# Optimization experiments

Measured on AMD Instinct MI355X. Metric: run time of the kernel, lower is better.

Reference implementation:

```python
import jax, jax.numpy as jnp
import numpy as np

NUM_EXPERTS = 64
TOP_K = 2
TEMPERATURE = 1.0
MOMENTUM = 0.9


def _l2norm(x, axis=-1):
    # torch F.normalize: x / max(||x||, eps)
    n = jnp.linalg.norm(x, axis=axis, keepdims=True)
    return x / jnp.maximum(n, 1e-12)


def setup_inputs() -> dict:
    key = jax.random.key(0)
    k1, k2 = jax.random.split(key)
    hidden_states = jax.random.normal(k1, (4, 4096, 2048), dtype=jnp.float32)
    centers = _l2norm(jax.random.normal(k2, (NUM_EXPERTS, 2048), dtype=jnp.float32))
    return {"hidden_states": hidden_states, "centers": centers}


def reference(hidden_states, centers):
    B, T, H = hidden_states.shape
    flat = hidden_states.reshape(-1, H).astype(jnp.float32)  # [N, H]
    N = flat.shape[0]

    # cosine-similarity logits
    reps_n = _l2norm(flat)
    centers_n = _l2norm(centers)
    temp = jnp.maximum(jnp.float32(TEMPERATURE), 1e-6)
    logits = (reps_n @ centers_n.T) / temp  # [N, E]

    probs = jax.nn.softmax(logits, axis=-1)
    top_w, top_ids = jax.lax.top_k(probs, TOP_K)  # [N, k]
    top_w = top_w / (jnp.sum(top_w, axis=-1, keepdims=True) + 1e-9)

    # EMA center update from top-1 routed expert (training+update path)
    route = top_ids[:, 0]  # [N]
    sums = jax.ops.segment_sum(flat, route, num_segments=NUM_EXPERTS)  # [E, H]
    counts = jax.ops.segment_sum(jnp.ones((N, 1), jnp.float32), route,
                                 num_segments=NUM_EXPERTS)  # [E, 1]
    means = sums / (counts + 1e-6)
    updated = _l2norm(MOMENTUM * centers + (1.0 - MOMENTUM) * means)
    new_centers = jnp.where(counts > 0, updated, centers)

    top_ids = top_ids.reshape(B, T, TOP_K)
    top_w = top_w.reshape(B, T, TOP_K)
    return top_ids, top_w, new_centers
```

## Files before the change

kernel.cpp:

```cpp
#include <hip/hip_runtime.h>
#include <math.h>

#define NTOK 16384
#define HDIM 2048
#define NEXP 64
#define KK   32
#define TAU  5e-5f
#define MAXB 2048
#define TB   16
#define KPAD 40
#define TPAD 20

typedef __attribute__((ext_vector_type(8))) short short8;
typedef __attribute__((ext_vector_type(4))) float f32x4;
typedef __attribute__((ext_vector_type(2))) unsigned int uint2v;


__global__ __launch_bounds__(256)
void zero_kernel(float* p, int n) {
  int i = blockIdx.x * 256 + threadIdx.x;
  if (i < n) p[i] = 0.0f;
}

__device__ __forceinline__ float block_reduce_sum(float v, float* red) {
  #pragma unroll
  for (int o = 32; o > 0; o >>= 1) v += __shfl_down(v, o, 64);
  int lane = threadIdx.x & 63;
  int wid  = threadIdx.x >> 6;
  if (lane == 0) red[wid] = v;
  __syncthreads();
  float s = red[0] + red[1] + red[2] + red[3];
  __syncthreads();
  return s;
}

__device__ __forceinline__ double block_reduce_sum_f64(double v, double* red) {
  const int tid = threadIdx.x;
  red[tid] = v;
  __syncthreads();
  if (tid < 128) red[tid] += red[tid + 128];
  __syncthreads();
  if (tid < 64)  red[tid] += red[tid + 64];
  __syncthreads();
  double s = 0.0;
  if (tid < 64) {
    s = red[tid];
    #pragma unroll
    for (int o = 32; o > 0; o >>= 1) s += __shfl_down(s, o, 64);
  }
  if (tid == 0) red[0] = s;
  __syncthreads();
  s = red[0];
  __syncthreads();
  return s;
}

__global__ __launch_bounds__(256)
void cnorm_kernel(const float* __restrict__ c, float* __restrict__ inv_nc) {
  __shared__ float red[4];
  int e = blockIdx.x;
  float ss = 0.f;
  #pragma unroll
  for (int j = 0; j < 8; ++j) {
    float v = c[e * HDIM + threadIdx.x + j * 256];
    ss += v * v;
  }
  float tot = block_reduce_sum(ss, red);
  if (threadIdx.x == 0) inv_nc[e] = 1.0f / fmaxf(sqrtf(tot), 1e-12f);
}

__global__ __launch_bounds__(256)
void cprep_kernel(const float* __restrict__ c, float* __restrict__ inv_nc,
                  float* __restrict__ bn, unsigned short* __restrict__ cbh,
                  unsigned short* __restrict__ cbl, int* __restrict__ zr,
                  int* __restrict__ cnt) {
  __shared__ float red[4];
  __shared__ double redd[256];
  __shared__ float s_nc;
  const int e = blockIdx.x;
  const int tid = threadIdx.x;
  if (e == 0 && tid < 128) zr[tid] = 0;
  if (e == 1 && tid < 64)  cnt[tid] = 0;
  const float* cr = c + (size_t)e * HDIM;
  float ss = 0.f;
  double acc = 0.0;
  #pragma unroll
  for (int j = 0; j < 8; ++j) {
    float v = cr[tid + j * 256];
    ss += v * v;
    double dv = (double)v;
    acc += dv * dv;
  }
  float tot = block_reduce_sum(ss, red);
  double cn = block_reduce_sum_f64(acc, redd);
  if (tid == 0) {
    inv_nc[e] = 1.0f / fmaxf(sqrtf(tot), 1e-12f);
    s_nc = (float)fmax(sqrt(cn), 1e-12);
  }
  __syncthreads();
  const double nc = (double)s_nc;
  #pragma unroll
  for (int j = 0; j < 8; ++j) {
    const int k = tid + j * 256;
    const float v = cr[k];
    bn[(size_t)e * HDIM + k] = (float)((double)v / nc);
    unsigned u = __float_as_uint(v);
    unsigned h = u & 0xffff0000u;
    float r = v - __uint_as_float(h);
    cbh[(size_t)e * HDIM + k] = (unsigned short)(u >> 16);
    cbl[(size_t)e * HDIM + k] = (unsigned short)(__float_as_uint(r) >> 16);
  }
}

__device__ __forceinline__ void cvt2(float v0, float v1, unsigned &hi, unsigned &lo) {
  unsigned u0 = __float_as_uint(v0);
  unsigned u1 = __float_as_uint(v1);
  unsigned h0 = u0 & 0xffff0000u;
  unsigned h1 = u1 & 0xffff0000u;
  float r0 = v0 - __uint_as_float(h0);
  float r1 = v1 - __uint_as_float(h1);
  hi = (u0 >> 16) | h1;
  lo = (__float_as_uint(r0) >> 16) | (__float_as_uint(r1) & 0xffff0000u);
}

__global__ __launch_bounds__(128)
void fused_kernel(const float* __restrict__ x,
                  const unsigned short* __restrict__ cbh,
                  const unsigned short* __restrict__ cbl,
                  const float* __restrict__ inv_nc,
                  float* __restrict__ out, int* __restrict__ route,
                  int* __restrict__ nflag, int* __restrict__ flags,
                  int* __restrict__ cursor, int* __restrict__ cnt,
                  int* __restrict__ bucket, int* __restrict__ posa) {
  __shared__ __align__(16) unsigned short Ah[2][TB][KPAD];
  __shared__ __align__(16) unsigned short Al[2][TB][KPAD];
  __shared__ __align__(16) unsigned short Bh[2][NEXP][KPAD];
  __shared__ __align__(16) unsigned short Bl[2][NEXP][KPAD];
  __shared__ float lg[NEXP][TPAD];
  __shared__ float xn_lds[TB];
  __shared__ float snc[NEXP];

  const int tid  = threadIdx.x;
  const int t0   = blockIdx.x * TB;
  const int sr   = tid >> 3;
  const int sq   = (tid & 7) * 4;
  const int er   = tid >> 1;
  const int eq   = (tid & 1) * 16;
  const int lane = tid & 63;
  const int w    = tid >> 6;
  const int eh   = w * 32;
  const int fr   = lane & 15;
  const int fk   = (lane >> 4) * 8;

  if (tid < NEXP) snc[tid] = inv_nc[tid];

  const float*          xptr = x   + (size_t)(t0 + sr) * HDIM + sq;
  const unsigned short* bh_p = cbh + (size_t)er * HDIM + eq;
  const unsigned short* bl_p = cbl + (size_t)er * HDIM + eq;

  f32x4 xp;
  short8 bh0r, bh1r, bl0r, bl1r;
  float nacc = 0.f;

  auto stage = [&](int b) {
    unsigned h01, l01, h23, l23;
    cvt2(xp.x, xp.y, h01, l01);
    cvt2(xp.z, xp.w, h23, l23);
    *(uint2v*)&Ah[b][sr][sq] = (uint2v){h01, h23};
    *(uint2v*)&Al[b][sr][sq] = (uint2v){l01, l23};
    nacc += xp.x*xp.x + xp.y*xp.y + xp.z*xp.z + xp.w*xp.w;
    *(short8*)&Bh[b][er][eq]     = bh0r;
    *(short8*)&Bh[b][er][eq + 8] = bh1r;
    *(short8*)&Bl[b][er][eq]     = bl0r;
    *(short8*)&Bl[b][er][eq + 8] = bl1r;
  };
  auto ldreg = [&](int it) {
    const int o = it * KK;
    xp   = *(const f32x4*)(xptr + o);
    bh0r = *(const short8*)(bh_p + o);
    bh1r = *(const short8*)(bh_p + o + 8);
    bl0r = *(const short8*)(bl_p + o);
    bl1r = *(const short8*)(bl_p + o + 8);
  };

  ldreg(0);
  stage(0);
  ldreg(1);
  __syncthreads();

  f32x4 acc0 = (f32x4){0.f, 0.f, 0.f, 0.f};
  f32x4 acc1 = (f32x4){0.f, 0.f, 0.f, 0.f};

  for (int it = 0; it < 64; ++it) {
    const int cur = it & 1;
    short8 ah  = *(const short8*)&Ah[cur][fr][fk];
    short8 al  = *(const short8*)&Al[cur][fr][fk];
    short8 bh0 = *(const short8*)&Bh[cur][eh + fr][fk];
    short8 bl0 = *(const short8*)&Bl[cur][eh + fr][fk];
    short8 bh1 = *(const short8*)&Bh[cur][eh + 16 + fr][fk];
    short8 bl1 = *(const short8*)&Bl[cur][eh + 16 + fr][fk];
    if (it < 63) {
      stage(cur ^ 1);
      if (it < 62) ldreg(it + 2);
    }
    acc0 = __builtin_amdgcn_mfma_f32_16x16x32_bf16(ah, bh0, acc0, 0, 0, 0);
    acc0 = __builtin_amdgcn_mfma_f32_16x16x32_bf16(ah, bl0, acc0, 0, 0, 0);
    acc0 = __builtin_amdgcn_mfma_f32_16x16x32_bf16(al, bh0, acc0, 0, 0, 0);
    acc1 = __builtin_amdgcn_mfma_f32_16x16x32_bf16(ah, bh1, acc1, 0, 0, 0);
    acc1 = __builtin_amdgcn_mfma_f32_16x16x32_bf16(ah, bl1, acc1, 0, 0, 0);
    acc1 = __builtin_amdgcn_mfma_f32_16x16x32_bf16(al, bh1, acc1, 0, 0, 0);
    __syncthreads();
  }

  float s = nacc;
  s += __shfl_xor(s, 1, 64);
  s += __shfl_xor(s, 2, 64);
  s += __shfl_xor(s, 4, 64);
  if ((tid & 7) == 0) xn_lds[sr] = s;

  const int tb = (lane >> 4) * 4;
  *(f32x4*)&lg[eh + fr][tb]      = acc0;
  *(f32x4*)&lg[eh + 16 + fr][tb] = acc1;
  __syncthreads();

  if (tid < TB) {
    const int t  = tid;
    const int tg = t0 + t;
    const float inv_nx = 1.0f / fmaxf(sqrtf(xn_lds[t]), 1e-12f);
    float m1 = -1e30f, m2 = -1e30f, m3 = -1e30f;
    int i1 = 0, i2 = 0;
    #pragma unroll
    for (int e = 0; e < NEXP; ++e) {
      float l = lg[e][t] * snc[e] * inv_nx;
      if (l > m1)      { m3 = m2; m2 = m1; i2 = i1; m1 = l; i1 = e; }
      else if (l > m2) { m3 = m2; m2 = l; i2 = e; }
      else if (l > m3) { m3 = l; }
    }
    float Z = 0.f;
    #pragma unroll
    for (int e = 0; e < NEXP; ++e)
      Z += expf(lg[e][t] * snc[e] * inv_nx - m1);
    const float p1w = 1.0f / Z;
    const float p2w = expf(m2 - m1) / Z;
    const float s2  = p1w + p2w + 1e-9f;
    out[tg * 2 + 0] = (float)i1;
    out[tg * 2 + 1] = (float)i2;
    out[2 * NTOK + tg * 2 + 0] = p1w / s2;
    out[2 * NTOK + tg * 2 + 1] = p2w / s2;
    route[tg] = i1;
    const int p = atomicAdd(&cursor[i1], 1);
    atomicAdd(&cnt[i1], 1);
    if (p < MAXB) bucket[i1 * MAXB + p] = tg;
    posa[tg] = p;
    if ((m1 - m2) < TAU || (m2 - m3) < TAU) {
      int idx = atomicAdd(nflag, 1);
      flags[idx] = tg;
    }
  }
}

__global__ __launch_bounds__(256)
void refine_np_kernel(const float* __restrict__ x, const float* __restrict__ bn,
                      float* __restrict__ out, int* __restrict__ route,
                      const int* __restrict__ nflag, const int* __restrict__ flags,
                      int* __restrict__ cursor, int* __restrict__ cnt,
                      int* __restrict__ bucket, int* __restrict__ posa) {
  __shared__ float a_lds[HDIM];
  __shared__ double redd[256];
  __shared__ float lf[NEXP];
  __shared__ float s_nx;
  const int tid  = threadIdx.x;
  const int lane = tid & 63;
  const int w    = tid >> 6;
  const int n = *nflag;
  for (int j = blockIdx.x; j < n; j += gridDim.x) {
    const int t = flags[j];
    const float* xr = x + (size_t)t * HDIM;
    double xacc = 0.0;
    #pragma unroll
    for (int i = 0; i < 8; ++i) {
      double v = (double)xr[tid + 256 * i];
      xacc += v * v;
    }
    double xn = block_reduce_sum_f64(xacc, redd);
    if (tid == 0) s_nx = (float)fmax(sqrt(xn), 1e-12);
    __syncthreads();
    const double nx = (double)s_nx;
    #pragma unroll
    for (int i = 0; i < 8; ++i) {
      int k = tid + 256 * i;
      a_lds[k] = (float)((double)xr[k] / nx);
    }
    __syncthreads();
    #pragma unroll 1
    for (int ei = 0; ei < 16; ++ei) {
      const int e = w * 16 + ei;
      const float* br = bn + (size_t)e * HDIM;
      double d = 0.0;
      #pragma unroll 8
      for (int i = 0; i < 32; ++i) {
        int k = lane + 64 * i;
        d += (double)a_lds[k] * (double)br[k];
      }
      #pragma unroll
      for (int o = 32; o > 0; o >>= 1) d += __shfl_down(d, o, 64);
      if (lane == 0) lf[e] = (float)d;
    }
    __syncthreads();
    if (tid == 0) {
      float m32 = lf[0];
      for (int ee = 1; ee < NEXP; ++ee) m32 = fmaxf(m32, lf[ee]);
      float ex[NEXP];
      for (int ee = 0; ee < NEXP; ++ee)
        ex[ee] = (float)exp((double)(lf[ee] - m32));
      float r[8];
      #pragma unroll
      for (int q = 0; q < 8; ++q) r[q] = ex[q];
      for (int i = 8; i < NEXP; i += 8)
        #pragma unroll
        for (int q = 0; q < 8; ++q) r[q] += ex[i + q];
      const float Z = ((r[0] + r[1]) + (r[2] + r[3])) + ((r[4] + r[5]) + (r[6] + r[7]));
      float p1 = -1.f, p2 = -1.f;
      int i1 = 0, i2 = 0;
      for (int ee = 0; ee < NEXP; ++ee) {
        float p = ex[ee] / Z;
        if (p > p1)      { p2 = p1; i2 = i1; p1 = p; i1 = ee; }
        else if (p > p2) { p2 = p; i2 = ee; }
      }
      const float s = (p1 + p2) + 1e-9f;
      out[t * 2 + 0] = (float)i1;
      out[t * 2 + 1] = (float)i2;
      out[2 * NTOK + t * 2 + 0] = p1 / s;
      out[2 * NTOK + t * 2 + 1] = p2 / s;
      const int old = route[t];
      if (i1 != old) {
        const int p_old = posa[t];
        if (p_old < MAXB) bucket[old * MAXB + p_old] = -1;
        atomicSub(&cnt[old], 1);
        const int p = atomicAdd(&cursor[i1], 1);
        atomicAdd(&cnt[i1], 1);
        if (p < MAXB) bucket[i1 * MAXB + p] = t;
        posa[t] = p;
        route[t] = i1;
      }
    }
    __syncthreads();
  }
}

__global__ __launch_bounds__(64)
void refine_np_slow(const float* __restrict__ x, const float* __restrict__ c,
                    float* __restrict__ out, int* __restrict__ route,
                    const int* __restrict__ nflag, const int* __restrict__ flags) {
  __shared__ float lf[NEXP];
  const int e = threadIdx.x;
  const int n = *nflag;
  for (int j = blockIdx.x; j < n; j += gridDim.x) {
    const int t = flags[j];
    const float* xr = x + (size_t)t * HDIM;
    const float* cr = c + (size_t)e * HDIM;
    double xn = 0.0, cn = 0.0;
    for (int k = 0; k < HDIM; ++k) {
      double xv = (double)xr[k];
      double cv = (double)cr[k];
      xn += xv * xv;
      cn += cv * cv;
    }
    const float nx32 = (float)fmax(sqrt(xn), 1e-12);
    const float nc32 = (float)fmax(sqrt(cn), 1e-12);
    double d = 0.0;
    for (int k = 0; k < HDIM; ++k) {
      float a = (float)((double)xr[k] / (double)nx32);
      float b = (float)((double)cr[k] / (double)nc32);
      d += (double)a * (double)b;
    }
    lf[e] = (float)d;
    __syncthreads();
    if (e == 0) {
      float m32 = lf[0];
      for (int ee = 1; ee < NEXP; ++ee) m32 = fmaxf(m32, lf[ee]);
      float ex[NEXP];
      for (int ee = 0; ee < NEXP; ++ee)
        ex[ee] = (float)exp((double)(lf[ee] - m32));
      float r[8];
      #pragma unroll
      for (int q = 0; q < 8; ++q) r[q] = ex[q];
      for (int i = 8; i < NEXP; i += 8)
        #pragma unroll
        for (int q = 0; q < 8; ++q) r[q] += ex[i + q];
      const float Z = ((r[0] + r[1]) + (r[2] + r[3])) + ((r[4] + r[5]) + (r[6] + r[7]));
      float p1 = -1.f, p2 = -1.f;
      int i1 = 0, i2 = 0;
      for (int ee = 0; ee < NEXP; ++ee) {
        float p = ex[ee] / Z;
        if (p > p1)      { p2 = p1; i2 = i1; p1 = p; i1 = ee; }
        else if (p > p2) { p2 = p; i2 = ee; }
      }
      const float s = (p1 + p2) + 1e-9f;
      out[t * 2 + 0] = (float)i1;
      out[t * 2 + 1] = (float)i2;
      out[2 * NTOK + t * 2 + 0] = p1 / s;
      out[2 * NTOK + t * 2 + 1] = p2 / s;
      route[t] = i1;
    }
    __syncthreads();
  }
}

__global__ __launch_bounds__(256)
void segsum_part(const float* __restrict__ x, const int* __restrict__ cursor,
                 const int* __restrict__ bucket, float* __restrict__ psum) {
  __shared__ f32x4 part[4][64];
  const int e   = blockIdx.x >> 5;
  const int hc  = (blockIdx.x >> 2) & 7;
  const int ts  = blockIdx.x & 3;
  const int hb  = hc * 256;
  const int tid = threadIdx.x;
  const int rg  = tid >> 6;
  const int cc  = tid & 63;
  int n = cursor[e];
  if (n > MAXB) n = MAXB;
  const int nq = (n + 3) >> 2;
  const int lo = ts * nq;
  const int hi = min(lo + nq, n);
  const int* bk = bucket + e * MAXB;
  f32x4 a = (f32x4){0.f, 0.f, 0.f, 0.f};
  #pragma unroll 4
  for (int i = lo + rg; i < hi; i += 4) {
    const int r = bk[i];
    if (r >= 0) a += *(const f32x4*)(x + (size_t)r * HDIM + hb + cc * 4);
  }
  part[rg][cc] = a;
  __syncthreads();
  if (tid < 64) {
    f32x4 s = part[0][tid] + part[1][tid] + part[2][tid] + part[3][tid];
    *(f32x4*)&psum[(size_t)(ts * NEXP + e) * HDIM + hb + tid * 4] = s;
  }
}

__global__ __launch_bounds__(256)
void finalize4_kernel(const float* __restrict__ c, const float* __restrict__ psum,
                      const int* __restrict__ counts, float* __restrict__ out) {
  __shared__ float red[4];
  const int e = blockIdx.x;
  const int tid = threadIdx.x;
  const float cnt = (float)counts[e];
  const float minv = 1.0f / (cnt + 1e-6f);
  float u[8], cv[8];
  float ss = 0.f;
  #pragma unroll
  for (int j = 0; j < 8; ++j) {
    int h = tid + j * 256;
    cv[j] = c[e * HDIM + h];
    float sm = psum[(size_t)(0 * NEXP + e) * HDIM + h]
             + psum[(size_t)(1 * NEXP + e) * HDIM + h]
             + psum[(size_t)(2 * NEXP + e) * HDIM + h]
             + psum[(size_t)(3 * NEXP + e) * HDIM + h];
    float mean = sm * minv;
    u[j] = 0.9f * cv[j] + 0.1f * mean;
    ss += u[j] * u[j];
  }
  float tot = block_reduce_sum(ss, red);
  float sc = 1.0f / fmaxf(sqrtf(tot), 1e-12f);
  const bool nz = cnt > 0.f;
  #pragma unroll
  for (int j = 0; j < 8; ++j) {
    int h = tid + j * 256;
    out[4 * NTOK + e * HDIM + h] = nz ? u[j] * sc : cv[j];
  }
}

__global__ __launch_bounds__(256)
void finalize_kernel(const float* __restrict__ c, const float* __restrict__ sums,
                     const int* __restrict__ counts, float* __restrict__ out) {
  __shared__ float red[4];
  const int e = blockIdx.x;
  const int tid = threadIdx.x;
  const float cnt = (float)counts[e];
  const float minv = 1.0f / (cnt + 1e-6f);
  float u[8], cv[8];
  float ss = 0.f;
  #pragma unroll
  for (int j = 0; j < 8; ++j) {
    int h = tid + j * 256;
    cv[j] = c[e * HDIM + h];
    float mean = sums[e * HDIM + h] * minv;
    u[j] = 0.9f * cv[j] + 0.1f * mean;
    ss += u[j] * u[j];
  }
  float tot = block_reduce_sum(ss, red);
  float sc = 1.0f / fmaxf(sqrtf(tot), 1e-12f);
  const bool nz = cnt > 0.f;
  #pragma unroll
  for (int j = 0; j < 8; ++j) {
    int h = tid + j * 256;
    out[4 * NTOK + e * HDIM + h] = nz ? u[j] * sc : cv[j];
  }
}

__global__ __launch_bounds__(256)
void router_kernel(const float* __restrict__ x, const float* __restrict__ c,
                   const float* __restrict__ inv_nc, float* __restrict__ out,
                   int* __restrict__ route, int* __restrict__ nflag,
                   int* __restrict__ flags) {
  __shared__ __align__(16) float xs[64][36];
  __shared__ float lgs[64][67];
  const int tid  = threadIdx.x;
  const int lane = tid & 63;
  const int w    = tid >> 6;
  const int t0   = blockIdx.x * 64;
  const int e0   = __builtin_amdgcn_readfirstlane(w * 16);
  const float* cb = c + (size_t)e0 * HDIM;
  const int st = tid >> 3;
  const int sk = (tid & 7) * 4;
  float acc[16];
  #pragma unroll
  for (int e = 0; e < 16; ++e) acc[e] = 0.f;
  float nacc = 0.f;
  float4 p0 = *(const float4*)&x[(size_t)(t0 + st)      * HDIM + sk];
  float4 p1 = *(const float4*)&x[(size_t)(t0 + st + 32) * HDIM + sk];
  for (int k0 = 0; k0 < HDIM; k0 += 32) {
    __syncthreads();
    *(float4*)&xs[st][sk]      = p0;
    *(float4*)&xs[st + 32][sk] = p1;
    __syncthreads();
    const int kn = k0 + 32;
    if (kn < HDIM) {
      p0 = *(const float4*)&x[(size_t)(t0 + st)      * HDIM + kn + sk];
      p1 = *(const float4*)&x[(size_t)(t0 + st + 32) * HDIM + kn + sk];
    }
    float a[32];
    #pragma unroll
    for (int j = 0; j < 32; j += 4) {
      float4 v = *(const float4*)&xs[lane][j];
      a[j] = v.x; a[j+1] = v.y; a[j+2] = v.z; a[j+3] = v.w;
    }
    if (w == 0) {
      #pragma unroll
      for (int j = 0; j < 32; ++j) nacc += a[j] * a[j];
    }
    #pragma unroll
    for (int e = 0; e < 16; ++e) {
      const float* br = cb + (size_t)e * HDIM + k0;
      #pragma unroll
      for (int j = 0; j < 32; j += 4) {
        float4 bv = *(const float4*)&br[j];
        acc[e] += a[j]*bv.x + a[j+1]*bv.y + a[j+2]*bv.z + a[j+3]*bv.w;
      }
    }
  }
  #pragma unroll
  for (int e = 0; e < 16; ++e) lgs[lane][e0 + e] = acc[e] * inv_nc[e0 + e];
  __syncthreads();
  if (w == 0) {
    const float inv_nx = 1.0f / fmaxf(sqrtf(nacc), 1e-12f);
    float m1 = -1e30f, m2 = -1e30f, m3 = -1e30f;
    int i1 = 0, i2 = 0;
    for (int e = 0; e < NEXP; ++e) {
      float l = lgs[lane][e] * inv_nx;
      if (l > m1)      { m3 = m2; m2 = m1; i2 = i1; m1 = l; i1 = e; }
      else if (l > m2) { m3 = m2; m2 = l; i2 = e; }
      else if (l > m3) { m3 = l; }
    }
    float Z = 0.f;
    for (int e = 0; e < NEXP; ++e) Z += expf(lgs[lane][e] * inv_nx - m1);
    const float p1w = 1.0f / Z;
    const float p2w = expf(m2 - m1) / Z;
    const float s   = p1w + p2w + 1e-9f;
    const int tg = t0 + lane;
    out[tg * 2 + 0] = (float)i1;
    out[tg * 2 + 1] = (float)i2;
    out[2 * NTOK + tg * 2 + 0] = p1w / s;
    out[2 * NTOK + tg * 2 + 1] = p2w / s;
    route[tg] = i1;
    if ((m1 - m2) < TAU || (m2 - m3) < TAU) {
      int idx = atomicAdd(nflag, 1);
      flags[idx] = tg;
    }
  }
}

__global__ __launch_bounds__(512)
void segsum_kernel(const float* __restrict__ x, const int* __restrict__ route,
                   float* __restrict__ sums, int* __restrict__ counts) {
  __shared__ float ls[NEXP * 256];
  __shared__ int lcnt[NEXP];
  const int tid  = threadIdx.x;
  const int lane = tid & 63;
  const int w    = tid >> 6;
  const int hc   = blockIdx.x & 7;
  const int tg   = blockIdx.x >> 3;
  const int hb   = hc * 256;
  #pragma unroll
  for (int i = 0; i < 32; ++i) ls[tid + i * 512] = 0.f;
  if (tid < NEXP) lcnt[tid] = 0;
  __syncthreads();
  const int tbase = tg * 512 + w * 64;
  #pragma unroll 4
  for (int i = 0; i < 64; ++i) {
    const int t = tbase + i;
    const int e = route[t];
    const float* xr = x + (size_t)t * HDIM + hb + lane;
    #pragma unroll
    for (int j = 0; j < 4; ++j)
      atomicAdd(&ls[e * 256 + lane + 64 * j], xr[64 * j]);
    if (hc == 0 && lane == 0) atomicAdd(&lcnt[e], 1);
  }
  __syncthreads();
  #pragma unroll
  for (int i = tid; i < NEXP * 256; i += 512) {
    const int e = i >> 8, h = i & 255;
    atomicAdd(&sums[e * HDIM + hb + h], ls[i]);
  }
  if (hc == 0 && tid < NEXP && lcnt[tid] > 0) atomicAdd(&counts[tid], lcnt[tid]);
}

extern "C" void kernel_launch(void* const* d_in, const int* in_sizes, int n_in,
                              void* d_out, int out_size, void* d_ws, size_t ws_size,
                              hipStream_t stream) {
  const float* x = (const float*)d_in[0];
  const float* c = (const float*)d_in[1];
  float* out = (float*)d_out;
  float* ws = (float*)d_ws;

  float* inv_nc = ws;
  int*   cursor = (int*)(ws + 64);
  int*   nflag  = (int*)(ws + 128);
  int*   route  = (int*)(ws + 192);
  int*   flags  = (int*)(ws + 16576);
  float* sums   = ws + 32960;
  float* bn     = ws + 164032;
  unsigned short* cbh = (unsigned short*)(ws + 295104);
  unsigned short* cbl = (unsigned short*)(ws + 360640);
  int*   bucket = (int*)(ws + 426176);
  float* psum   = ws + 557248;
  int*   posa   = (int*)(ws + 1081536);
  int*   cnt    = (int*)(ws + 1097920);

  const size_t NEED = 1097984ull * 4ull;
  if (ws_size >= NEED) {
    cprep_kernel<<<NEXP, 256, 0, stream>>>(c, inv_nc, bn, cbh, cbl, cursor, cnt);
    fused_kernel<<<NTOK / TB, 128, 0, stream>>>(x, cbh, cbl, inv_nc, out, route,
                                                nflag, flags, cursor, cnt, bucket, posa);
    refine_np_kernel<<<512, 256, 0, stream>>>(x, bn, out, route, nflag, flags,
                                              cursor, cnt, bucket, posa);
    segsum_part<<<2048, 256, 0, stream>>>(x, cursor, bucket, psum);
    finalize4_kernel<<<NEXP, 256, 0, stream>>>(c, psum, cnt, out);
  } else {
    zero_kernel<<<1, 256, 0, stream>>>(ws + 64, 128);
    zero_kernel<<<512, 256, 0, stream>>>(sums, 131072);
    cnorm_kernel<<<NEXP, 256, 0, stream>>>(c, inv_nc);
    router_kernel<<<NTOK / 64, 256, 0, stream>>>(x, c, inv_nc, out, route, nflag, flags);
    refine_np_slow<<<1024, 64, 0, stream>>>(x, c, out, route, nflag, flags);
    segsum_kernel<<<256, 512, 0, stream>>>(x, route, sums, cursor);
    finalize_kernel<<<NEXP, 256, 0, stream>>>(c, sums, cursor, out);
  }
}
```

Measured before the change: 310.3 us.

## Split routing GEMM into split-K partial kernel plus separate softmax/top-k kernel

The fused GEMM+softmax kernel (16-token tiles, full K loop) is replaced by a split-K GEMM that processes 64-token by 64-expert tiles over 256-wide K slices across 2048 blocks, writing partial logits and partial squared norms to workspace. A new softmax2 kernel sums the 8 partials per token and does the top-k, softmax, bucketing and flagging. The aim is more parallelism and more reuse of each centers tile per block. The cost is extra global traffic for the partial logits (8×64×16384 floats), an extra launch, and the loss of double buffering in the GEMM loop.

```diff
diff --git a/kernel.cpp b/kernel.cpp
--- a/kernel.cpp
+++ b/kernel.cpp
@@ -7,9 +7,8 @@
 #define KK   32
 #define TAU  5e-5f
 #define MAXB 2048
-#define TB   16
-#define KPAD 40
-#define TPAD 20
+#define KP2  40
+#define LTS2 68
 
 typedef __attribute__((ext_vector_type(8))) short short8;
 typedef __attribute__((ext_vector_type(4))) float f32x4;
@@ -123,139 +122,168 @@
   lo = (__float_as_uint(r0) >> 16) | (__float_as_uint(r1) & 0xffff0000u);
 }
 
-__global__ __launch_bounds__(128)
-void fused_kernel(const float* __restrict__ x,
-                  const unsigned short* __restrict__ cbh,
-                  const unsigned short* __restrict__ cbl,
-                  const float* __restrict__ inv_nc,
-                  float* __restrict__ out, int* __restrict__ route,
-                  int* __restrict__ nflag, int* __restrict__ flags,
-                  int* __restrict__ cursor, int* __restrict__ cnt,
-                  int* __restrict__ bucket, int* __restrict__ posa) {
-  __shared__ __align__(16) unsigned short Ah[2][TB][KPAD];
-  __shared__ __align__(16) unsigned short Al[2][TB][KPAD];
-  __shared__ __align__(16) unsigned short Bh[2][NEXP][KPAD];
-  __shared__ __align__(16) unsigned short Bl[2][NEXP][KPAD];
-  __shared__ float lg[NEXP][TPAD];
-  __shared__ float xn_lds[TB];
-  __shared__ float snc[NEXP];
+__global__ __launch_bounds__(256)
+void gemm_part(const float* __restrict__ x,
+               const unsigned short* __restrict__ cbh,
+               const unsigned short* __restrict__ cbl,
+               float* __restrict__ lp, float* __restrict__ xnp) {
+  __shared__ __align__(16) unsigned short smem[10240];
+  unsigned short (*Ah)[KP2] = (unsigned short (*)[KP2])(smem);
+  unsigned short (*Al)[KP2] = (unsigned short (*)[KP2])(smem + 2560);
+  unsigned short (*Bh)[KP2] = (unsigned short (*)[KP2])(smem + 5120);
+  unsigned short (*Bl)[KP2] = (unsigned short (*)[KP2])(smem + 7680);
 
   const int tid  = threadIdx.x;
-  const int t0   = blockIdx.x * TB;
-  const int sr   = tid >> 3;
-  const int sq   = (tid & 7) * 4;
-  const int er   = tid >> 1;
-  const int eq   = (tid & 1) * 16;
+  const int mt   = blockIdx.x >> 3;
+  const int ks   = blockIdx.x & 7;
+  const int t0   = mt * 64;
+  const int kb   = ks * 256;
+  const int sr   = tid >> 2;
+  const int sq   = (tid & 3) * 8;
   const int lane = tid & 63;
   const int w    = tid >> 6;
-  const int eh   = w * 32;
+  const int tw   = (w & 1) * 32;
+  const int ew   = (w >> 1) * 32;
   const int fr   = lane & 15;
   const int fk   = (lane >> 4) * 8;
 
-  if (tid < NEXP) snc[tid] = inv_nc[tid];
-
-  const float*          xptr = x   + (size_t)(t0 + sr) * HDIM + sq;
-  const unsigned short* bh_p = cbh + (size_t)er * HDIM + eq;
-  const unsigned short* bl_p = cbl + (size_t)er * HDIM + eq;
-
-  f32x4 xp;
-  short8 bh0r, bh1r, bl0r, bl1r;
+  const float*          xrow  = x   + (size_t)(t0 + sr) * HDIM + kb + sq;
+  const unsigned short* bhrow = cbh + (size_t)sr * HDIM + kb + sq;
+  const unsigned short* blrow = cbl + (size_t)sr * HDIM + kb + sq;
+
+  f32x4 xp0, xp1;
+  short8 bhp, blp;
   float nacc = 0.f;
 
-  auto stage = [&](int b) {
-    unsigned h01, l01, h23, l23;
-    cvt2(xp.x, xp.y, h01, l01);
-    cvt2(xp.z, xp.w, h23, l23);
-    *(uint2v*)&Ah[b][sr][sq] = (uint2v){h01, h23};
-    *(uint2v*)&Al[b][sr][sq] = (uint2v){l01, l23};
-    nacc += xp.x*xp.x + xp.y*xp.y + xp.z*xp.z + xp.w*xp.w;
-    *(short8*)&Bh[b][er][eq]     = bh0r;
-    *(short8*)&Bh[b][er][eq + 8] = bh1r;
-    *(short8*)&Bl[b][er][eq]     = bl0r;
-    *(short8*)&Bl[b][er][eq + 8] = bl1r;
-  };
-  auto ldreg = [&](int it) {
-    const int o = it * KK;
-    xp   = *(const f32x4*)(xptr + o);
-    bh0r = *(const short8*)(bh_p + o);
-    bh1r = *(const short8*)(bh_p + o + 8);
-    bl0r = *(const short8*)(bl_p + o);
-    bl1r = *(const short8*)(bl_p + o + 8);
-  };
-
-  ldreg(0);
-  stage(0);
-  ldreg(1);
-  __syncthreads();
-
-  f32x4 acc0 = (f32x4){0.f, 0.f, 0.f, 0.f};
-  f32x4 acc1 = (f32x4){0.f, 0.f, 0.f, 0.f};
-
-  for (int it = 0; it < 64; ++it) {
-    const int cur = it & 1;
-    short8 ah  = *(const short8*)&Ah[cur][fr][fk];
-    short8 al  = *(const short8*)&Al[cur][fr][fk];
-    short8 bh0 = *(const short8*)&Bh[cur][eh + fr][fk];
-    short8 bl0 = *(const short8*)&Bl[cur][eh + fr][fk];
-    short8 bh1 = *(const short8*)&Bh[cur][eh + 16 + fr][fk];
-    short8 bl1 = *(const short8*)&Bl[cur][eh + 16 + fr][fk];
-    if (it < 63) {
-      stage(cur ^ 1);
-      if (it < 62) ldreg(it + 2);
-    }
-    acc0 = __builtin_amdgcn_mfma_f32_16x16x32_bf16(ah, bh0, acc0, 0, 0, 0);
-    acc0 = __builtin_amdgcn_mfma_f32_16x16x32_bf16(ah, bl0, acc0, 0, 0, 0);
-    acc0 = __builtin_amdgcn_mfma_f32_16x16x32_bf16(al, bh0, acc0, 0, 0, 0);
-    acc1 = __builtin_amdgcn_mfma_f32_16x16x32_bf16(ah, bh1, acc1, 0, 0, 0);
-    acc1 = __builtin_amdgcn_mfma_f32_16x16x32_bf16(ah, bl1, acc1, 0, 0, 0);
-    acc1 = __builtin_amdgcn_mfma_f32_16x16x32_bf16(al, bh1, acc1, 0, 0, 0);
-    __syncthreads();
+  xp0 = *(const f32x4*)(xrow);
+  xp1 = *(const f32x4*)(xrow + 4);
+  bhp = *(const short8*)(bhrow);
+  blp = *(const short8*)(blrow);
+
+  f32x4 acc[2][2];
+  #pragma unroll
+  for (int mi = 0; mi < 2; ++mi)
+    #pragma unroll
+    for (int ni = 0; ni < 2; ++ni)
+      acc[mi][ni] = (f32x4){0.f, 0.f, 0.f, 0.f};
+
+  for (int it = 0; it < 8; ++it) {
+    __syncthreads();
+    {
+      unsigned h01, l01, h23, l23, h45, l45, h67, l67;
+      cvt2(xp0.x, xp0.y, h01, l01);
+      cvt2(xp0.z, xp0.w, h23, l23);
+      cvt2(xp1.x, xp1.y, h45, l45);
+      cvt2(xp1.z, xp1.w, h67, l67);
+      *(uint2v*)&Ah[sr][sq]     = (uint2v){h01, h23};
+      *(uint2v*)&Ah[sr][sq + 4] = (uint2v){h45, h67};
+      *(uint2v*)&Al[sr][sq]     = (uint2v){l01, l23};
+      *(uint2v*)&Al[sr][sq + 4] = (uint2v){l45, l67};
+      nacc += xp0.x*xp0.x + xp0.y*xp0.y + xp0.z*xp0.z + xp0.w*xp0.w
+            + xp1.x*xp1.x + xp1.y*xp1.y + xp1.z*xp1.z + xp1.w*xp1.w;
+      *(short8*)&Bh[sr][sq] = bhp;
+      *(short8*)&Bl[sr][sq] = blp;
+    }
+    __syncthreads();
+    if (it < 7) {
+      const int o = (it + 1) * KK;
+      xp0 = *(const f32x4*)(xrow + o);
+      xp1 = *(const f32x4*)(xrow + o + 4);
+      bhp = *(const short8*)(bhrow + o);
+      blp = *(const short8*)(blrow + o);
+    }
+    short8 ah0 = *(const short8*)&Ah[tw + fr][fk];
+    short8 ah1 = *(const short8*)&Ah[tw + 16 + fr][fk];
+    short8 al0 = *(const short8*)&Al[tw + fr][fk];
+    short8 al1 = *(const short8*)&Al[tw + 16 + fr][fk];
+    #pragma unroll
+    for (int ni = 0; ni < 2; ++ni) {
+      short8 bh = *(const short8*)&Bh[ew + ni * 16 + fr][fk];
+      short8 bl = *(const short8*)&Bl[ew + ni * 16 + fr][fk];
+      acc[0][ni] = __builtin_amdgcn_mfma_f32_16x16x32_bf16(ah0, bh, acc[0][ni], 0, 0, 0);
+      acc[0][ni] = __builtin_amdgcn_mfma_f32_16x16x32_bf16(ah0, bl, acc[0][ni], 0, 0, 0);
+      acc[0][ni] = __builtin_amdgcn_mfma_f32_16x16x32_bf16(al0, bh, acc[0][ni], 0, 0, 0);
+      acc[1][ni] = __builtin_amdgcn_mfma_f32_16x16x32_bf16(ah1, bh, acc[1][ni], 0, 0, 0);
+      acc[1][ni] = __builtin_amdgcn_mfma_f32_16x16x32_bf16(ah1, bl, acc[1][ni], 0, 0, 0);
+      acc[1][ni] = __builtin_amdgcn_mfma_f32_16x16x32_bf16(al1, bh, acc[1][ni], 0, 0, 0);
+    }
   }
 
   float s = nacc;
   s += __shfl_xor(s, 1, 64);
   s += __shfl_xor(s, 2, 64);
-  s += __shfl_xor(s, 4, 64);
-  if ((tid & 7) == 0) xn_lds[sr] = s;
-
-  const int tb = (lane >> 4) * 4;
-  *(f32x4*)&lg[eh + fr][tb]      = acc0;
-  *(f32x4*)&lg[eh + 16 + fr][tb] = acc1;
-  __syncthreads();
-
-  if (tid < TB) {
-    const int t  = tid;
-    const int tg = t0 + t;
-    const float inv_nx = 1.0f / fmaxf(sqrtf(xn_lds[t]), 1e-12f);
-    float m1 = -1e30f, m2 = -1e30f, m3 = -1e30f;
-    int i1 = 0, i2 = 0;
-    #pragma unroll
-    for (int e = 0; e < NEXP; ++e) {
-      float l = lg[e][t] * snc[e] * inv_nx;
-      if (l > m1)      { m3 = m2; m2 = m1; i2 = i1; m1 = l; i1 = e; }
-      else if (l > m2) { m3 = m2; m2 = l; i2 = e; }
-      else if (l > m3) { m3 = l; }
-    }
-    float Z = 0.f;
-    #pragma unroll
-    for (int e = 0; e < NEXP; ++e)
-      Z += expf(lg[e][t] * snc[e] * inv_nx - m1);
-    const float p1w = 1.0f / Z;
-    const float p2w = expf(m2 - m1) / Z;
-    const float s2  = p1w + p2w + 1e-9f;
-    out[tg * 2 + 0] = (float)i1;
-    out[tg * 2 + 1] = (float)i2;
-    out[2 * NTOK + tg * 2 + 0] = p1w / s2;
-    out[2 * NTOK + tg * 2 + 1] = p2w / s2;
-    route[tg] = i1;
-    const int p = atomicAdd(&cursor[i1], 1);
-    atomicAdd(&cnt[i1], 1);
-    if (p < MAXB) bucket[i1 * MAXB + p] = tg;
-    posa[tg] = p;
-    if ((m1 - m2) < TAU || (m2 - m3) < TAU) {
-      int idx = atomicAdd(nflag, 1);
-      flags[idx] = tg;
-    }
+  if ((tid & 3) == 0) xnp[ks * NTOK + t0 + sr] = s;
+
+  __syncthreads();
+  float* lt = (float*)smem;
+  const int tloc = tw + (lane >> 4) * 4;
+  #pragma unroll
+  for (int mi = 0; mi < 2; ++mi)
+    #pragma unroll
+    for (int ni = 0; ni < 2; ++ni)
+      *(f32x4*)&lt[(ew + ni * 16 + fr) * LTS2 + tloc + mi * 16] = acc[mi][ni];
+  __syncthreads();
+  #pragma unroll
+  for (int n = 0; n < 16; ++n) {
+    const int f = tid + n * 256;
+    const int e = f >> 6;
+    const int t = f & 63;
+    lp[(size_t)(ks * NEXP + e) * NTOK + t0 + t] = lt[e * LTS2 + t];
+  }
+}
+
+__global__ __launch_bounds__(64)
+void softmax2_kernel(const float* __restrict__ lp, const float* __restrict__ xnp,
+                     const float* __restrict__ inv_nc, float* __restrict__ out,
+                     int* __restrict__ route, int* __restrict__ nflag,
+                     int* __restrict__ flags, int* __restrict__ cursor,
+                     int* __restrict__ cnt, int* __restrict__ bucket,
+                     int* __restrict__ posa) {
+  __shared__ float snc[NEXP];
+  const int tid = threadIdx.x;
+  snc[tid] = inv_nc[tid];
+  __syncthreads();
+  const int t = blockIdx.x * 64 + tid;
+  float xs2 = 0.f;
+  #pragma unroll
+  for (int k = 0; k < 8; ++k) xs2 += xnp[k * NTOK + t];
+  const float inv_nx = 1.0f / fmaxf(sqrtf(xs2), 1e-12f);
+  float lv[NEXP];
+  #pragma unroll
+  for (int e = 0; e < NEXP; ++e) {
+    float a = 0.f;
+    #pragma unroll
+    for (int k = 0; k < 8; ++k)
+      a += lp[(size_t)(k * NEXP + e) * NTOK + t];
+    lv[e] = a * snc[e] * inv_nx;
+  }
+  float m1 = -1e30f, m2 = -1e30f, m3 = -1e30f;
+  int i1 = 0, i2 = 0;
+  #pragma unroll
+  for (int e = 0; e < NEXP; ++e) {
+    float l = lv[e];
+    if (l > m1)      { m3 = m2; m2 = m1; i2 = i1; m1 = l; i1 = e; }
+    else if (l > m2) { m3 = m2; m2 = l; i2 = e; }
+    else if (l > m3) { m3 = l; }
+  }
+  float Z = 0.f;
+  #pragma unroll
+  for (int e = 0; e < NEXP; ++e) Z += expf(lv[e] - m1);
+  const float p1w = 1.0f / Z;
+  const float p2w = expf(m2 - m1) / Z;
+  const float s2  = p1w + p2w + 1e-9f;
+  out[t * 2 + 0] = (float)i1;
+  out[t * 2 + 1] = (float)i2;
+  out[2 * NTOK + t * 2 + 0] = p1w / s2;
+  out[2 * NTOK + t * 2 + 1] = p2w / s2;
+  route[t] = i1;
+  const int p = atomicAdd(&cursor[i1], 1);
+  atomicAdd(&cnt[i1], 1);
+  if (p < MAXB) bucket[i1 * MAXB + p] = t;
+  posa[t] = p;
+  if ((m1 - m2) < TAU || (m2 - m3) < TAU) {
+    int idx = atomicAdd(nflag, 1);
+    flags[idx] = t;
   }
 }
 
@@ -636,12 +664,15 @@
   float* psum   = ws + 557248;
   int*   posa   = (int*)(ws + 1081536);
   int*   cnt    = (int*)(ws + 1097920);
-
-  const size_t NEED = 1097984ull * 4ull;
+  float* lp     = ws + 1097984;
+  float* xnp    = ws + 9486592;
+
+  const size_t NEED = 9617664ull * 4ull;
   if (ws_size >= NEED) {
     cprep_kernel<<<NEXP, 256, 0, stream>>>(c, inv_nc, bn, cbh, cbl, cursor, cnt);
-    fused_kernel<<<NTOK / TB, 128, 0, stream>>>(x, cbh, cbl, inv_nc, out, route,
-                                                nflag, flags, cursor, cnt, bucket, posa);
+    gemm_part<<<2048, 256, 0, stream>>>(x, cbh, cbl, lp, xnp);
+    softmax2_kernel<<<NTOK / 64, 64, 0, stream>>>(lp, xnp, inv_nc, out, route,
+                                                  nflag, flags, cursor, cnt, bucket, posa);
     refine_np_kernel<<<512, 256, 0, stream>>>(x, bn, out, route, nflag, flags,
                                               cursor, cnt, bucket, posa);
     segsum_part<<<2048, 256, 0, stream>>>(x, cursor, bucket, psum);
```

Result: slower. 339.1 us (+9.3%).
